# Kernel tuning notes

Measured on AMD Instinct MI355X. Metric: run time of the kernel, lower is better.

The kernel has to match this reference:

```python
import jax, jax.numpy as jnp
import numpy as np
from math import factorial

MAXL = 5
TAUS = [8, 8, 8, 8, 8, 8]
OUT_TAUS = [8, 8, 8, 8, 8, 8]
BM_EPS = 1e-5
BATCH = 1024


def _cg_coeff(l1, l2, l, m1, m2, m):
    # Standard Clebsch-Gordan coefficient <l1 m1 l2 m2 | l m> (Racah formula).
    if m1 + m2 != m:
        return 0.0
    f = factorial
    pre = ((2 * l + 1) * f(l + l1 - l2) * f(l - l1 + l2) * f(l1 + l2 - l) / f(l1 + l2 + l + 1)) ** 0.5
    pre *= (f(l + m) * f(l - m) * f(l1 - m1) * f(l1 + m1) * f(l2 - m2) * f(l2 + m2)) ** 0.5
    s = 0.0
    for k in range(0, l1 + l2 - l + 1):
        ds = [k, l1 + l2 - l - k, l1 - m1 - k, l2 + m2 - k, l - l2 + m1 + k, l - l1 - m2 + k]
        if min(ds) < 0:
            continue
        d = 1.0
        for v in ds:
            d *= f(v)
        s += (-1.0) ** k / d
    return pre * s


def _cg_block(l1, l2, l):
    C = np.zeros((2 * l + 1, 2 * l1 + 1, 2 * l2 + 1), dtype=np.float32)
    for m in range(-l, l + 1):
        for m1 in range(-l1, l1 + 1):
            m2 = m - m1
            if -l2 <= m2 <= l2:
                C[m + l, m1 + l1, m2 + l2] = _cg_coeff(l1, l2, l, m1, m2, m)
    return C


# Triple enumeration order matches cal_middle_taus (l1 outer, l2, then l).
TRIPLES = []
for _l1 in range(MAXL + 1):
    for _l2 in range(_l1 + 1):
        for _l in range(_l1 - _l2, min(_l1 + _l2, MAXL) + 1):
            TRIPLES.append((_l1, _l2, _l))
CG_BLOCKS = [jnp.asarray(_cg_block(*t)) for t in TRIPLES]

MIDDLE_TAUS = np.zeros(MAXL + 1, dtype=np.int64)
for (_l1, _l2, _l) in TRIPLES:
    MIDDLE_TAUS[_l] += TAUS[_l1] * TAUS[_l2]
IN_LEN = int(sum(TAUS[l] * (2 * l + 1) for l in range(MAXL + 1)))    # 288
OUT_LEN = int(sum(OUT_TAUS[l] * (2 * l + 1) for l in range(MAXL + 1)))  # 288
WLEN = int(sum(OUT_TAUS[l] * int(MIDDLE_TAUS[l]) for l in range(MAXL + 1)))  # 35328
STD_LEN = int(MIDDLE_TAUS.sum())  # 4416


def _forward(activations, weights, moving_std):
    B = activations.shape[0]
    act = activations[..., 0] + 1j * activations[..., 1]  # [B, IN_LEN] complex64
    # split into per-degree blocks F[l]: [B, tau_l, 2l+1]
    F = []
    st = 0
    for l in range(MAXL + 1):
        n = TAUS[l] * (2 * l + 1)
        F.append(act[:, st:st + n].reshape(B, TAUS[l], 2 * l + 1))
        st += n
    # CG tensor product: one fragment per (l1,l2,l) triple, grouped by output degree l
    mids = [[] for _ in range(MAXL + 1)]
    for (l1, l2, l), C in zip(TRIPLES, CG_BLOCKS):
        frag = jnp.einsum('mac,bta,bsc->btsm', C.astype(act.dtype), F[l1], F[l2])
        mids[l].append(frag.reshape(B, TAUS[l1] * TAUS[l2], 2 * l + 1))
    # per-fragment batchnorm (divide by running std) + per-degree complex mixing
    outs = []
    so = 0
    wo = 0
    for l in range(MAXL + 1):
        mid = jnp.concatenate(mids[l], axis=1)  # [B, middle_taus[l], 2l+1]
        nt = int(MIDDLE_TAUS[l])
        std = moving_std[so:so + nt]
        so += nt
        mid = mid / (std + BM_EPS)[None, :, None]
        nw = OUT_TAUS[l] * nt
        wl = weights[wo:wo + nw]
        wo += nw
        Wc = (wl[:, 0] + 1j * wl[:, 1]).reshape(OUT_TAUS[l], nt)
        out = jnp.einsum('ot,btm->bom', Wc, mid)  # [B, out_taus[l], 2l+1]
        outs.append(out.reshape(B, OUT_TAUS[l] * (2 * l + 1)))
    oc = jnp.concatenate(outs, axis=1)  # [B, OUT_LEN] complex
    return jnp.stack([oc.real, oc.imag], axis=-1)  # [B, OUT_LEN, 2]


def setup_inputs() -> dict:
    key = jax.random.key(0)
    k1, k2, k3 = jax.random.split(key, 3)
    activations = jax.random.normal(k1, (BATCH, IN_LEN, 2), dtype=jnp.float32)
    weights = 0.05 * jax.random.uniform(k2, (WLEN, 2), dtype=jnp.float32)
    moving_std = 0.1 + 0.9 * jax.random.uniform(k3, (STD_LEN,), dtype=jnp.float32)
    return {"activations": activations, "weights": weights, "moving_std": moving_std}


def reference(activations, weights, moving_std):
    return _forward(activations, weights, moving_std)
```

## Files before the change

kernel.cpp:

```cpp
#include <hip/hip_runtime.h>
#include <hip/hip_bf16.h>
#include <utility>


constexpr int NTRIP = 69;
constexpr int NL    = 6;
constexpr int BATCH = 1024;
constexpr int ROW   = 288;
constexpr int MID_LDS = 4224;

struct Meta {
    int tl1[NTRIP], tl2[NTRIP], tll[NTRIP];
    int tf1[NTRIP], tf2[NTRIP];
    int ttloc[NTRIP];
    int tcg[NTRIP];
    int trip_of_l[NL][16];
    int ntrips[NL];
    int mid_tau[NL], std_off[NL], w_off[NL], f_l[NL];
    int nch[NL];
    int ch_start[NL][2], ch_cnt[NL][2];
    int wave_of[NL][16];
    int cg_total;
};

constexpr Meta build_meta() {
    Meta m{};
    int fl[NL] = {};
    {
        int acc = 0;
        for (int l = 0; l < NL; l++) { fl[l] = acc; m.f_l[l] = acc; acc += 8 * (2 * l + 1); }
    }
    int idx = 0, cgo = 0;
    for (int l1 = 0; l1 <= 5; l1++)
        for (int l2 = 0; l2 <= l1; l2++) {
            int lmax = (l1 + l2 < 5) ? (l1 + l2) : 5;
            for (int l = l1 - l2; l <= lmax; l++) {
                m.tl1[idx] = l1; m.tl2[idx] = l2; m.tll[idx] = l;
                m.tf1[idx] = fl[l1]; m.tf2[idx] = fl[l2];
                m.ttloc[idx] = 64 * m.ntrips[l];
                m.trip_of_l[l][m.ntrips[l]] = idx;
                m.ntrips[l]++;
                m.tcg[idx] = cgo;
                cgo += (2 * l + 1) * (2 * l1 + 1) * (2 * l2 + 1);
                idx++;
            }
        }
    m.cg_total = cgo;
    int so = 0, wo = 0;
    for (int l = 0; l < NL; l++) {
        m.mid_tau[l] = 64 * m.ntrips[l];
        m.std_off[l] = so; so += m.mid_tau[l];
        m.w_off[l]   = wo; wo += 8 * m.mid_tau[l];
    }
    for (int l = 0; l < NL; l++) {
        const int TW = 2 * l + 1;
        const int maxslot = MID_LDS / (64 * TW);
        const int ntl = m.ntrips[l];
        const int nch = (ntl + maxslot - 1) / maxslot;
        m.nch[l] = nch;
        int done = 0;
        for (int c = 0; c < nch; c++) {
            int cnt = (ntl - done + (nch - c) - 1) / (nch - c);
            m.ch_start[l][c] = done; m.ch_cnt[l][c] = cnt; done += cnt;
        }
        for (int c = 0; c < nch; c++) {
            const int s0 = m.ch_start[l][c], cnt = m.ch_cnt[l][c];
            int cost[16] = {}; bool asg[16] = {};
            for (int i = 0; i < cnt; i++) {
                int trip = m.trip_of_l[l][s0 + i];
                int l1 = m.tl1[trip], l2 = m.tl2[trip];
                int tc = 0;
                for (int mi = 0; mi < TW; mi++) {
                    int base = mi - l;
                    int lo = base + l1 - l2; if (lo < 0) lo = 0;
                    int hi = base + l1 + l2; if (hi > 2 * l1) hi = 2 * l1;
                    tc += hi - lo + 1;
                }
                cost[i] = tc * 6 + (2 * l1 + 1 + 2 * l2 + 1) * 2;
            }
            int load[4] = {};
            for (int k = 0; k < cnt; k++) {
                int best = -1, bc = -1;
                for (int i = 0; i < cnt; i++)
                    if (!asg[i] && cost[i] > bc) { bc = cost[i]; best = i; }
                asg[best] = true;
                int wsel = 0;
                for (int w2 = 1; w2 < 4; w2++) if (load[w2] < load[wsel]) wsel = w2;
                m.wave_of[l][s0 + best] = wsel;
                load[wsel] += bc;
            }
        }
    }
    return m;
}

constexpr Meta MT = build_meta();
static_assert(MT.cg_total == 24367, "cg table size");
constexpr int CG_TOTAL = MT.cg_total;
constexpr int WLEN     = 35328;
static_assert(MT.w_off[5] + 8 * MT.mid_tau[5] == WLEN, "wlen");
static_assert(MT.std_off[5] + MT.mid_tau[5] == 4416, "stdlen");

template <int... Is, class F>
__device__ __forceinline__ void static_for_impl(std::integer_sequence<int, Is...>, F&& f) {
    (f(std::integral_constant<int, Is>{}), ...);
}
template <int N, class F>
__device__ __forceinline__ void static_for(F&& f) {
    static_for_impl(std::make_integer_sequence<int, N>{}, (F&&)f);
}

__device__ __forceinline__ double dfact(int n) {
    double r = 1.0;
    for (int i = 2; i <= n; i++) r *= (double)i;
    return r;
}

__global__ void cg_init(float* __restrict__ cg) {
    int i = blockIdx.x * 256 + threadIdx.x;
    if (i >= CG_TOTAL) return;
    int trip = 0;
    for (int k = 1; k < NTRIP; k++) if (MT.tcg[k] <= i) trip = k;
    const int l1 = MT.tl1[trip], l2 = MT.tl2[trip], l = MT.tll[trip];
    const int n1 = 2 * l1 + 1, n2 = 2 * l2 + 1;
    int rel = i - MT.tcg[trip];
    int mi = rel / (n1 * n2);
    int r2 = rel - mi * n1 * n2;
    int ai = r2 / n2;
    int ci = r2 - ai * n2;
    int m = mi - l, m1 = ai - l1, m2 = ci - l2;
    float v = 0.f;
    if (m1 + m2 == m) {
        double pre = sqrt((double)(2 * l + 1) * dfact(l + l1 - l2) * dfact(l - l1 + l2) *
                          dfact(l1 + l2 - l) / dfact(l1 + l2 + l + 1));
        pre *= sqrt(dfact(l + m) * dfact(l - m) * dfact(l1 - m1) * dfact(l1 + m1) *
                    dfact(l2 - m2) * dfact(l2 + m2));
        double s = 0.0;
        for (int k = 0; k <= l1 + l2 - l; k++) {
            int d0 = k, d1 = l1 + l2 - l - k, d2 = l1 - m1 - k;
            int d3 = l2 + m2 - k, d4 = l - l2 + m1 + k, d5 = l - l1 - m2 + k;
            if (d0 < 0 || d1 < 0 || d2 < 0 || d3 < 0 || d4 < 0 || d5 < 0) continue;
            double den = dfact(d0) * dfact(d1) * dfact(d2) * dfact(d3) * dfact(d4) * dfact(d5);
            s += ((k & 1) ? -1.0 : 1.0) / den;
        }
        v = (float)(pre * s);
    }
    cg[i] = v;
}

__global__ void w_init(const float2* __restrict__ w,
                       const float* __restrict__ stdv,
                       float2* __restrict__ wp) {
    int i = blockIdx.x * 256 + threadIdx.x;
    if (i >= WLEN) return;
    int l = 0;
    for (int k = 1; k < NL; k++) if (MT.w_off[k] <= i) l = k;
    int rel = i - MT.w_off[l];
    int T = rel % MT.mid_tau[l];
    float inv = 1.0f / (stdv[MT.std_off[l] + T] + 1e-5f);
    float2 wv = w[i];
    wp[i] = make_float2(wv.x * inv, wv.y * inv);
}

template <int L>
__device__ __forceinline__ void process_l(int b, int tid,
                                          const float2* __restrict__ F,
                                          float2* __restrict__ mid,
                                          const float* __restrict__ cg,
                                          const float2* __restrict__ wp,
                                          float2* __restrict__ out) {
    constexpr int TW  = 2 * L + 1;
    constexpr int NCH = MT.nch[L];
    constexpr int NT  = MT.mid_tau[L];

    const int wid  = tid >> 6;
    const int lane = tid & 63;
    const int t = lane >> 3, s = lane & 7;
    const int g  = tid >> 5;
    const int hl = tid & 31;

    float2 acc[TW];
#pragma unroll
    for (int i = 0; i < TW; i++) acc[i] = make_float2(0.f, 0.f);

    static_for<NCH>([&](auto CHc) {
        constexpr int CH  = decltype(CHc)::value;
        constexpr int S0  = MT.ch_start[L][CH];
        constexpr int CNT = MT.ch_cnt[L][CH];
        constexpr int CT  = CNT * 64;
        static_assert(CT * TW <= MID_LDS, "chunk fits");

        __syncthreads();

        static_for<CNT>([&](auto SIc) {
            constexpr int SI   = S0 + decltype(SIc)::value;
            constexpr int TRIP = MT.trip_of_l[L][SI];
            constexpr int L1   = MT.tl1[TRIP];
            constexpr int L2v  = MT.tl2[TRIP];
            constexpr int N1   = 2 * L1 + 1, N2 = 2 * L2v + 1;
            if (MT.wave_of[L][SI] == wid) {
                const float2* F1 = F + MT.tf1[TRIP] + t * N1;
                const float2* F2 = F + MT.tf2[TRIP] + s * N2;
                float2 f1[N1], f2[N2];
#pragma unroll
                for (int i = 0; i < N1; i++) f1[i] = F1[i];
#pragma unroll
                for (int i = 0; i < N2; i++) f2[i] = F2[i];
                const int Tloc = (MT.ttloc[TRIP] - S0 * 64) + lane;
                static_for<TW>([&](auto MIc) {
                    constexpr int MI   = decltype(MIc)::value;
                    constexpr int BASE = MI - L;
                    constexpr int LO_  = BASE + L1 - L2v;
                    constexpr int LO   = LO_ < 0 ? 0 : LO_;
                    constexpr int HI_  = BASE + L1 + L2v;
                    constexpr int HI   = HI_ > 2 * L1 ? 2 * L1 : HI_;
                    float re = 0.f, im = 0.f;
                    static_for<HI - LO + 1>([&](auto Kc) {
                        constexpr int AI = LO + decltype(Kc)::value;
                        constexpr int CI = BASE + L1 + L2v - AI;
                        const float cv = cg[MT.tcg[TRIP] + MI * N1 * N2 + AI * N2 + CI];
                        const float2 a = f1[AI], c2 = f2[CI];
                        re = fmaf(cv, fmaf(-a.y, c2.y, a.x * c2.x), re);
                        im = fmaf(cv, fmaf(a.y, c2.x, a.x * c2.y), im);
                    });
                    mid[MI * CT + Tloc] = make_float2(re, im);
                });
            }
        });
        __syncthreads();

        const float2* W = wp + MT.w_off[L] + g * NT + S0 * 64;
        for (int T = hl * 2; T < CT; T += 64) {
            const float4 wv = *reinterpret_cast<const float4*>(W + T);
#pragma unroll
            for (int mi = 0; mi < TW; mi++) {
                const float4 mv = *reinterpret_cast<const float4*>(mid + mi * CT + T);
                acc[mi].x = fmaf(wv.x, mv.x, fmaf(-wv.y, mv.y,
                             fmaf(wv.z, mv.z, fmaf(-wv.w, mv.w, acc[mi].x))));
                acc[mi].y = fmaf(wv.x, mv.y, fmaf(wv.y, mv.x,
                             fmaf(wv.z, mv.w, fmaf(wv.w, mv.z, acc[mi].y))));
            }
        }
    });

#pragma unroll
    for (int off = 16; off >= 1; off >>= 1) {
#pragma unroll
        for (int mi = 0; mi < TW; mi++) {
            acc[mi].x += __shfl_xor(acc[mi].x, off, 64);
            acc[mi].y += __shfl_xor(acc[mi].y, off, 64);
        }
    }
    if (hl == 0) {
        float2* orow = out + (size_t)b * ROW + MT.f_l[L] + g * TW;
#pragma unroll
        for (int mi = 0; mi < TW; mi++) orow[mi] = acc[mi];
    }
}

__global__ __launch_bounds__(256, 4) void fup_main(const float2* __restrict__ act,
                                                   const float* __restrict__ cg,
                                                   const float2* __restrict__ wp,
                                                   float2* __restrict__ out) {
    __shared__ float2 F[ROW];
    __shared__ __align__(16) float2 mid[MID_LDS];
    const int b = blockIdx.x;
    const int tid = threadIdx.x;
    const float2* arow = act + (size_t)b * ROW;
    for (int i = tid; i < ROW; i += 256) F[i] = arow[i];
    process_l<0>(b, tid, F, mid, cg, wp, out);
    process_l<1>(b, tid, F, mid, cg, wp, out);
    process_l<2>(b, tid, F, mid, cg, wp, out);
    process_l<3>(b, tid, F, mid, cg, wp, out);
    process_l<4>(b, tid, F, mid, cg, wp, out);
    process_l<5>(b, tid, F, mid, cg, wp, out);
}

extern "C" void kernel_launch(void* const* d_in, const int* in_sizes, int n_in,
                              void* d_out, int out_size, void* d_ws, size_t ws_size,
                              hipStream_t stream) {
    const float2* act  = (const float2*)d_in[0];
    const float2* wts  = (const float2*)d_in[1];
    const float*  stdv = (const float*)d_in[2];
    float2* out = (float2*)d_out;

    float*  cg = (float*)d_ws;
    float2* wp = (float2*)((char*)d_ws + (size_t)24368 * 4);

    hipLaunchKernelGGL(cg_init, dim3((CG_TOTAL + 255) / 256), dim3(256), 0, stream, cg);
    hipLaunchKernelGGL(w_init,  dim3((WLEN + 255) / 256),     dim3(256), 0, stream,
                       wts, stdv, wp);
    hipLaunchKernelGGL(fup_main, dim3(BATCH), dim3(256), 0, stream, act, cg, wp, out);
}
```

Measured before the change: 137.8 us.

## Bake Clebsch-Gordan coefficients as constexpr and give each wave two output channels

Clebsch-Gordan coefficients are now computed at compile time and folded into the unrolled tensor-product code, and zero coefficients are skipped with if constexpr. This removes the cg_init kernel launch and the global loads of the coefficient table. The weight contraction now has each wave compute two output channels (wid and wid+4) over the full 64-lane stride, so every LDS load of mid feeds two accumulators. A cross-half shuffle then merges the two results before reduction. The risks are higher register pressure from doubling the accumulators and longer compile times from the large constexpr evaluation.

```diff
diff --git a/kernel.cpp b/kernel.cpp
--- a/kernel.cpp
+++ b/kernel.cpp
@@ -13,14 +13,12 @@
     int tl1[NTRIP], tl2[NTRIP], tll[NTRIP];
     int tf1[NTRIP], tf2[NTRIP];
     int ttloc[NTRIP];
-    int tcg[NTRIP];
     int trip_of_l[NL][16];
     int ntrips[NL];
     int mid_tau[NL], std_off[NL], w_off[NL], f_l[NL];
     int nch[NL];
     int ch_start[NL][2], ch_cnt[NL][2];
     int wave_of[NL][16];
-    int cg_total;
 };
 
 constexpr Meta build_meta() {
@@ -30,7 +28,7 @@
         int acc = 0;
         for (int l = 0; l < NL; l++) { fl[l] = acc; m.f_l[l] = acc; acc += 8 * (2 * l + 1); }
     }
-    int idx = 0, cgo = 0;
+    int idx = 0;
     for (int l1 = 0; l1 <= 5; l1++)
         for (int l2 = 0; l2 <= l1; l2++) {
             int lmax = (l1 + l2 < 5) ? (l1 + l2) : 5;
@@ -40,12 +38,9 @@
                 m.ttloc[idx] = 64 * m.ntrips[l];
                 m.trip_of_l[l][m.ntrips[l]] = idx;
                 m.ntrips[l]++;
-                m.tcg[idx] = cgo;
-                cgo += (2 * l + 1) * (2 * l1 + 1) * (2 * l2 + 1);
                 idx++;
             }
         }
-    m.cg_total = cgo;
     int so = 0, wo = 0;
     for (int l = 0; l < NL; l++) {
         m.mid_tau[l] = 64 * m.ntrips[l];
@@ -95,11 +90,36 @@
 }
 
 constexpr Meta MT = build_meta();
-static_assert(MT.cg_total == 24367, "cg table size");
-constexpr int CG_TOTAL = MT.cg_total;
-constexpr int WLEN     = 35328;
+constexpr int WLEN = 35328;
 static_assert(MT.w_off[5] + 8 * MT.mid_tau[5] == WLEN, "wlen");
 static_assert(MT.std_off[5] + MT.mid_tau[5] == 4416, "stdlen");
+
+constexpr double cfact(int n) {
+    double r = 1.0;
+    for (int i = 2; i <= n; i++) r *= (double)i;
+    return r;
+}
+constexpr double csqrt(double x) {
+    double g = x > 1.0 ? x : 1.0;
+    for (int i = 0; i < 100; i++) g = 0.5 * (g + x / g);
+    return g;
+}
+constexpr float cg_coeff(int l1, int l2, int l, int m1, int m2, int m) {
+    if (m1 + m2 != m) return 0.0f;
+    double pre = csqrt((double)(2 * l + 1) * cfact(l + l1 - l2) * cfact(l - l1 + l2) *
+                       cfact(l1 + l2 - l) / cfact(l1 + l2 + l + 1));
+    pre *= csqrt(cfact(l + m) * cfact(l - m) * cfact(l1 - m1) * cfact(l1 + m1) *
+                 cfact(l2 - m2) * cfact(l2 + m2));
+    double s = 0.0;
+    for (int k = 0; k <= l1 + l2 - l; k++) {
+        int d0 = k, d1 = l1 + l2 - l - k, d2 = l1 - m1 - k;
+        int d3 = l2 + m2 - k, d4 = l - l2 + m1 + k, d5 = l - l1 - m2 + k;
+        if (d0 < 0 || d1 < 0 || d2 < 0 || d3 < 0 || d4 < 0 || d5 < 0) continue;
+        double den = cfact(d0) * cfact(d1) * cfact(d2) * cfact(d3) * cfact(d4) * cfact(d5);
+        s += ((k & 1) ? -1.0 : 1.0) / den;
+    }
+    return (float)(pre * s);
+}
 
 template <int... Is, class F>
 __device__ __forceinline__ void static_for_impl(std::integer_sequence<int, Is...>, F&& f) {
@@ -108,44 +128,6 @@
 template <int N, class F>
 __device__ __forceinline__ void static_for(F&& f) {
     static_for_impl(std::make_integer_sequence<int, N>{}, (F&&)f);
-}
-
-__device__ __forceinline__ double dfact(int n) {
-    double r = 1.0;
-    for (int i = 2; i <= n; i++) r *= (double)i;
-    return r;
-}
-
-__global__ void cg_init(float* __restrict__ cg) {
-    int i = blockIdx.x * 256 + threadIdx.x;
-    if (i >= CG_TOTAL) return;
-    int trip = 0;
-    for (int k = 1; k < NTRIP; k++) if (MT.tcg[k] <= i) trip = k;
-    const int l1 = MT.tl1[trip], l2 = MT.tl2[trip], l = MT.tll[trip];
-    const int n1 = 2 * l1 + 1, n2 = 2 * l2 + 1;
-    int rel = i - MT.tcg[trip];
-    int mi = rel / (n1 * n2);
-    int r2 = rel - mi * n1 * n2;
-    int ai = r2 / n2;
-    int ci = r2 - ai * n2;
-    int m = mi - l, m1 = ai - l1, m2 = ci - l2;
-    float v = 0.f;
-    if (m1 + m2 == m) {
-        double pre = sqrt((double)(2 * l + 1) * dfact(l + l1 - l2) * dfact(l - l1 + l2) *
-                          dfact(l1 + l2 - l) / dfact(l1 + l2 + l + 1));
-        pre *= sqrt(dfact(l + m) * dfact(l - m) * dfact(l1 - m1) * dfact(l1 + m1) *
-                    dfact(l2 - m2) * dfact(l2 + m2));
-        double s = 0.0;
-        for (int k = 0; k <= l1 + l2 - l; k++) {
-            int d0 = k, d1 = l1 + l2 - l - k, d2 = l1 - m1 - k;
-            int d3 = l2 + m2 - k, d4 = l - l2 + m1 + k, d5 = l - l1 - m2 + k;
-            if (d0 < 0 || d1 < 0 || d2 < 0 || d3 < 0 || d4 < 0 || d5 < 0) continue;
-            double den = dfact(d0) * dfact(d1) * dfact(d2) * dfact(d3) * dfact(d4) * dfact(d5);
-            s += ((k & 1) ? -1.0 : 1.0) / den;
-        }
-        v = (float)(pre * s);
-    }
-    cg[i] = v;
 }
 
 __global__ void w_init(const float2* __restrict__ w,
@@ -166,7 +148,6 @@
 __device__ __forceinline__ void process_l(int b, int tid,
                                           const float2* __restrict__ F,
                                           float2* __restrict__ mid,
-                                          const float* __restrict__ cg,
                                           const float2* __restrict__ wp,
                                           float2* __restrict__ out) {
     constexpr int TW  = 2 * L + 1;
@@ -176,12 +157,10 @@
     const int wid  = tid >> 6;
     const int lane = tid & 63;
     const int t = lane >> 3, s = lane & 7;
-    const int g  = tid >> 5;
-    const int hl = tid & 31;
-
-    float2 acc[TW];
-#pragma unroll
-    for (int i = 0; i < TW; i++) acc[i] = make_float2(0.f, 0.f);
+
+    float2 acc0[TW], acc1[TW];
+#pragma unroll
+    for (int i = 0; i < TW; i++) { acc0[i] = make_float2(0.f, 0.f); acc1[i] = make_float2(0.f, 0.f); }
 
     static_for<NCH>([&](auto CHc) {
         constexpr int CH  = decltype(CHc)::value;
@@ -218,10 +197,12 @@
                     static_for<HI - LO + 1>([&](auto Kc) {
                         constexpr int AI = LO + decltype(Kc)::value;
                         constexpr int CI = BASE + L1 + L2v - AI;
-                        const float cv = cg[MT.tcg[TRIP] + MI * N1 * N2 + AI * N2 + CI];
-                        const float2 a = f1[AI], c2 = f2[CI];
-                        re = fmaf(cv, fmaf(-a.y, c2.y, a.x * c2.x), re);
-                        im = fmaf(cv, fmaf(a.y, c2.x, a.x * c2.y), im);
+                        constexpr float cv = cg_coeff(L1, L2v, L, AI - L1, CI - L2v, BASE);
+                        if constexpr (cv != 0.0f) {
+                            const float2 a = f1[AI], c2 = f2[CI];
+                            re = fmaf(cv, fmaf(-a.y, c2.y, a.x * c2.x), re);
+                            im = fmaf(cv, fmaf(a.y, c2.x, a.x * c2.y), im);
+                        }
                     });
                     mid[MI * CT + Tloc] = make_float2(re, im);
                 });
@@ -229,37 +210,50 @@
         });
         __syncthreads();
 
-        const float2* W = wp + MT.w_off[L] + g * NT + S0 * 64;
-        for (int T = hl * 2; T < CT; T += 64) {
-            const float4 wv = *reinterpret_cast<const float4*>(W + T);
+        const float2* W0 = wp + MT.w_off[L] + wid * NT + S0 * 64;
+        const float2* W1 = wp + MT.w_off[L] + (wid + 4) * NT + S0 * 64;
+        for (int T = lane * 2; T < CT; T += 128) {
+            const float4 w0 = *reinterpret_cast<const float4*>(W0 + T);
+            const float4 w1 = *reinterpret_cast<const float4*>(W1 + T);
 #pragma unroll
             for (int mi = 0; mi < TW; mi++) {
                 const float4 mv = *reinterpret_cast<const float4*>(mid + mi * CT + T);
-                acc[mi].x = fmaf(wv.x, mv.x, fmaf(-wv.y, mv.y,
-                             fmaf(wv.z, mv.z, fmaf(-wv.w, mv.w, acc[mi].x))));
-                acc[mi].y = fmaf(wv.x, mv.y, fmaf(wv.y, mv.x,
-                             fmaf(wv.z, mv.w, fmaf(wv.w, mv.z, acc[mi].y))));
+                acc0[mi].x = fmaf(w0.x, mv.x, fmaf(-w0.y, mv.y,
+                              fmaf(w0.z, mv.z, fmaf(-w0.w, mv.w, acc0[mi].x))));
+                acc0[mi].y = fmaf(w0.x, mv.y, fmaf(w0.y, mv.x,
+                              fmaf(w0.z, mv.w, fmaf(w0.w, mv.z, acc0[mi].y))));
+                acc1[mi].x = fmaf(w1.x, mv.x, fmaf(-w1.y, mv.y,
+                              fmaf(w1.z, mv.z, fmaf(-w1.w, mv.w, acc1[mi].x))));
+                acc1[mi].y = fmaf(w1.x, mv.y, fmaf(w1.y, mv.x,
+                              fmaf(w1.z, mv.w, fmaf(w1.w, mv.z, acc1[mi].y))));
             }
         }
     });
 
-#pragma unroll
-    for (int off = 16; off >= 1; off >>= 1) {
-#pragma unroll
-        for (int mi = 0; mi < TW; mi++) {
-            acc[mi].x += __shfl_xor(acc[mi].x, off, 64);
-            acc[mi].y += __shfl_xor(acc[mi].y, off, 64);
-        }
-    }
-    if (hl == 0) {
-        float2* orow = out + (size_t)b * ROW + MT.f_l[L] + g * TW;
-#pragma unroll
-        for (int mi = 0; mi < TW; mi++) orow[mi] = acc[mi];
+    const bool lo = (lane < 32);
+    float2 red[TW];
+#pragma unroll
+    for (int mi = 0; mi < TW; mi++) {
+        float gx = lo ? acc1[mi].x : acc0[mi].x;
+        float gy = lo ? acc1[mi].y : acc0[mi].y;
+        float rx = (lo ? acc0[mi].x : acc1[mi].x) + __shfl_xor(gx, 32, 64);
+        float ry = (lo ? acc0[mi].y : acc1[mi].y) + __shfl_xor(gy, 32, 64);
+#pragma unroll
+        for (int off = 16; off >= 1; off >>= 1) {
+            rx += __shfl_xor(rx, off, 64);
+            ry += __shfl_xor(ry, off, 64);
+        }
+        red[mi] = make_float2(rx, ry);
+    }
+    if (lane == 0 || lane == 32) {
+        const int o = wid + (lo ? 0 : 4);
+        float2* orow = out + (size_t)b * ROW + MT.f_l[L] + o * TW;
+#pragma unroll
+        for (int mi = 0; mi < TW; mi++) orow[mi] = red[mi];
     }
 }
 
 __global__ __launch_bounds__(256, 4) void fup_main(const float2* __restrict__ act,
-                                                   const float* __restrict__ cg,
                                                    const float2* __restrict__ wp,
                                                    float2* __restrict__ out) {
     __shared__ float2 F[ROW];
@@ -268,12 +262,12 @@
     const int tid = threadIdx.x;
     const float2* arow = act + (size_t)b * ROW;
     for (int i = tid; i < ROW; i += 256) F[i] = arow[i];
-    process_l<0>(b, tid, F, mid, cg, wp, out);
-    process_l<1>(b, tid, F, mid, cg, wp, out);
-    process_l<2>(b, tid, F, mid, cg, wp, out);
-    process_l<3>(b, tid, F, mid, cg, wp, out);
-    process_l<4>(b, tid, F, mid, cg, wp, out);
-    process_l<5>(b, tid, F, mid, cg, wp, out);
+    process_l<0>(b, tid, F, mid, wp, out);
+    process_l<1>(b, tid, F, mid, wp, out);
+    process_l<2>(b, tid, F, mid, wp, out);
+    process_l<3>(b, tid, F, mid, wp, out);
+    process_l<4>(b, tid, F, mid, wp, out);
+    process_l<5>(b, tid, F, mid, wp, out);
 }
 
 extern "C" void kernel_launch(void* const* d_in, const int* in_sizes, int n_in,
@@ -284,11 +278,9 @@
     const float*  stdv = (const float*)d_in[2];
     float2* out = (float2*)d_out;
 
-    float*  cg = (float*)d_ws;
-    float2* wp = (float2*)((char*)d_ws + (size_t)24368 * 4);
-
-    hipLaunchKernelGGL(cg_init, dim3((CG_TOTAL + 255) / 256), dim3(256), 0, stream, cg);
-    hipLaunchKernelGGL(w_init,  dim3((WLEN + 255) / 256),     dim3(256), 0, stream,
+    float2* wp = (float2*)d_ws;
+
+    hipLaunchKernelGGL(w_init, dim3((WLEN + 255) / 256), dim3(256), 0, stream,
                        wts, stdv, wp);
-    hipLaunchKernelGGL(fup_main, dim3(BATCH), dim3(256), 0, stream, act, cg, wp, out);
-}
+    hipLaunchKernelGGL(fup_main, dim3(BATCH), dim3(256), 0, stream, act, wp, out);
+}
```

After: 115.2 us. -16.4%, faster.
